# Performance work log

Measured on AMD Instinct MI355X. Metric: run time of the kernel, lower is better.

## Reference

```python
import jax, jax.numpy as jnp
import numpy as np

IMG = 1024       # original image resolution implied by (1024 - 1) normalization
STRIDE = 16
TEMP = 0.1
EPS = 1e-12      # F.normalize eps


def setup_inputs() -> dict:
    key = jax.random.key(0)
    k1, k2, k3, k4, k5 = jax.random.split(key, 5)
    B, C, Hf, Wf, N = 32, 256, 64, 64, 128
    feats_src = jax.random.normal(k1, (B, C, Hf, Wf), dtype=jnp.float32)
    feats_trg = jax.random.normal(k2, (B, C, Hf, Wf), dtype=jnp.float32)
    kps_src = jax.random.uniform(k3, (B, N, 2), dtype=jnp.float32) * (IMG - 1)
    kps_trg = jax.random.uniform(k4, (B, N, 2), dtype=jnp.float32) * (IMG - 1)
    kps_mask = jax.random.randint(k5, (B, N), 0, 2, dtype=jnp.int32)
    return {"feats_src": feats_src, "feats_trg": feats_trg,
            "kps_src": kps_src, "kps_trg": kps_trg, "kps_mask": kps_mask}


def _l2norm_c(x):
    # F.normalize(x, dim=1): x / max(||x||_2, eps) along channel dim
    n = jnp.sqrt(jnp.sum(x * x, axis=1, keepdims=True))
    return x / jnp.maximum(n, EPS)


def _bilinear_sample(feats, kps):
    # feats: [B,C,Hf,Wf]; kps: [B,N,2] pixel coords in [0, IMG-1]
    # Equivalent to F.grid_sample(align_corners=True, bilinear) with
    # grid = kps/(IMG-1)*2-1 -> pixel coords kps/(IMG-1)*(size-1).
    B, C, Hf, Wf = feats.shape
    x = kps[..., 0] / (IMG - 1) * (Wf - 1)  # [B,N]
    y = kps[..., 1] / (IMG - 1) * (Hf - 1)
    x0 = jnp.clip(jnp.floor(x), 0, Wf - 1).astype(jnp.int32)
    y0 = jnp.clip(jnp.floor(y), 0, Hf - 1).astype(jnp.int32)
    x1 = jnp.clip(x0 + 1, 0, Wf - 1)
    y1 = jnp.clip(y0 + 1, 0, Hf - 1)
    fx = x - x0.astype(x.dtype)
    fy = y - y0.astype(y.dtype)
    ft = jnp.transpose(feats, (0, 2, 3, 1))      # [B,Hf,Wf,C]
    bb = jnp.arange(B)[:, None]                  # [B,1] broadcasts to [B,N]
    g = lambda yy, xx: ft[bb, yy, xx]            # [B,N,C]
    wa = ((1 - fx) * (1 - fy))[..., None]
    wb = ((1 - fx) * fy)[..., None]
    wc = (fx * (1 - fy))[..., None]
    wd = (fx * fy)[..., None]
    return wa * g(y0, x0) + wb * g(y1, x0) + wc * g(y0, x1) + wd * g(y1, x1)


def reference(feats_src, feats_trg, kps_src, kps_trg, kps_mask):
    B, C, Hf, Wf = feats_src.shape
    N = kps_src.shape[1]
    fs = _l2norm_c(feats_src)
    ftg = _l2norm_c(feats_trg)

    # Query features sampled at source keypoints: [B,N,C]
    q = _bilinear_sample(fs, kps_src)

    # Logits over all target spatial positions: [B,N,Hf*Wf]
    trg_flat = ftg.reshape(B, C, Hf * Wf)
    logits = jnp.einsum('bnc,bcm->bnm', q, trg_flat) / TEMP

    # Bilinear soft targets at target keypoints (feature-grid coords)
    gx = kps_trg[..., 0] / STRIDE
    gy = kps_trg[..., 1] / STRIDE
    x0 = jnp.clip(jnp.floor(gx), 0, Wf - 1).astype(jnp.int32)
    x1 = jnp.clip(x0 + 1, 0, Wf - 1)
    y0 = jnp.clip(jnp.floor(gy), 0, Hf - 1).astype(jnp.int32)
    y1 = jnp.clip(y0 + 1, 0, Hf - 1)
    x0f, x1f = x0.astype(gx.dtype), x1.astype(gx.dtype)
    y0f, y1f = y0.astype(gy.dtype), y1.astype(gy.dtype)
    wa = (x1f - gx) * (y1f - gy)
    wb = (x1f - gx) * (gy - y0f)
    wc = (gx - x0f) * (y1f - gy)
    wd = (gx - x0f) * (gy - y0f)

    m = (kps_mask != 0).astype(logits.dtype)     # [B,N]
    w = jnp.stack([wa, wb, wc, wd], axis=-1) * m[..., None]   # [B,N,4]
    idx = jnp.stack([y0 * Wf + x0, y1 * Wf + x0,
                     y0 * Wf + x1, y1 * Wf + x1], axis=-1)    # [B,N,4]
    bb = jnp.arange(B)[:, None, None]
    nn = jnp.arange(N)[None, :, None]
    soft_targets = jnp.zeros_like(logits).at[bb, nn, idx].add(w)

    log_probs = jax.nn.log_softmax(logits, axis=-1)
    loss = -(soft_targets * log_probs).sum(axis=-1)           # [B,N]
    denom = jnp.maximum(m.sum(), 1.0)
    return (loss * m).sum() / denom
```

## Files before the change

### kernel.cpp

```cpp
#include <hip/hip_runtime.h>
#include <math.h>

#define B_    32
#define C_    256
#define HF    64
#define WF    64
#define M_    4096
#define N_    128
#define IMGM1 1023.0f
#define TEMP_ 0.1f
#define EPS_  1e-12f
#define NCH   32
#define SAS   40

typedef __attribute__((ext_vector_type(8))) short short8;
typedef __attribute__((ext_vector_type(4))) float floatx4;

__device__ __forceinline__ unsigned short f2bf(float x) {
  unsigned int u = __float_as_uint(x);
  u += 0x7fffu + ((u >> 16) & 1u);
  return (unsigned short)(u >> 16);
}
__device__ __forceinline__ float bf2f(unsigned short h) {
  return __uint_as_float(((unsigned int)h) << 16);
}
__device__ __forceinline__ float wave_sum(float v) {
#pragma unroll
  for (int off = 32; off; off >>= 1) v += __shfl_down(v, off, 64);
  return v;
}

__device__ __forceinline__ void src_geom(float kx, float ky, int& x0, int& y0,
                                         int& x1, int& y1, float& fx, float& fy) {
  const float x = kx / IMGM1 * (float)(WF - 1);
  const float y = ky / IMGM1 * (float)(HF - 1);
  x0 = (int)fminf(fmaxf(floorf(x), 0.f), 63.f);
  y0 = (int)fminf(fmaxf(floorf(y), 0.f), 63.f);
  x1 = min(x0 + 1, 63);
  y1 = min(y0 + 1, 63);
  fx = x - (float)x0;
  fy = y - (float)y0;
}

__global__ __launch_bounds__(256) void k1a_stage(const float* __restrict__ fs,
                                                 const float* __restrict__ kps,
                                                 ushort* __restrict__ corner,
                                                 float* __restrict__ ssqg) {
  const int cg = blockIdx.x, b = blockIdx.y, t = threadIdx.x;
  const int c0 = cg * 2;
  __shared__ __align__(16) float plane[2 * M_];
  __shared__ float4 ssq2[256];

  const float4* src = (const float4*)(fs + ((size_t)(b * C_ + c0)) * M_);
  float4* dst = (float4*)plane;
#pragma unroll
  for (int i = 0; i < 8; i++) dst[t + 256 * i] = src[t + 256 * i];
  __syncthreads();

  const int n = t & 127, p = t >> 7;
  const int c = c0 + p;
  const float kx = kps[((size_t)b * N_ + n) * 2 + 0];
  const float ky = kps[((size_t)b * N_ + n) * 2 + 1];
  int x0, y0, x1, y1; float fx, fy;
  src_geom(kx, ky, x0, y0, x1, y1, fx, fy);

  const float* pl = plane + p * M_;
  const float f00 = pl[y0 * WF + x0];
  const float f10 = pl[y1 * WF + x0];
  const float f01 = pl[y0 * WF + x1];
  const float f11 = pl[y1 * WF + x1];

  ushort4 cr;
  cr.x = f2bf(f00); cr.y = f2bf(f10); cr.z = f2bf(f01); cr.w = f2bf(f11);
  *(ushort4*)&corner[(((size_t)b * C_ + c) * N_ + n) * 4] = cr;

  ssq2[t] = make_float4(f00 * f00, f10 * f10, f01 * f01, f11 * f11);
  __syncthreads();
  if (t < 128) {
    const float4 a = ssq2[t], bq = ssq2[t + 128];
    float* g = ssqg + ((size_t)b * N_ + t) * 4;
    atomicAdd(g + 0, a.x + bq.x);
    atomicAdd(g + 1, a.y + bq.y);
    atomicAdd(g + 2, a.z + bq.z);
    atomicAdd(g + 3, a.w + bq.w);
  }
}

__global__ __launch_bounds__(256) void k1b_combine(const ushort* __restrict__ corner,
                                                   const float* __restrict__ ssqg,
                                                   const float* __restrict__ kps,
                                                   ushort* __restrict__ qbf) {
  const int n = blockIdx.x, b = blockIdx.y, c = threadIdx.x;
  const float kx = kps[((size_t)b * N_ + n) * 2 + 0];
  const float ky = kps[((size_t)b * N_ + n) * 2 + 1];
  int x0, y0, x1, y1; float fx, fy;
  src_geom(kx, ky, x0, y0, x1, y1, fx, fy);
  const float wa = (1.f - fx) * (1.f - fy), wb = (1.f - fx) * fy;
  const float wc = fx * (1.f - fy), wd = fx * fy;

  const float4 sq = *(const float4*)&ssqg[((size_t)b * N_ + n) * 4];
  const float r0 = 1.f / fmaxf(sqrtf(sq.x), EPS_);
  const float r1 = 1.f / fmaxf(sqrtf(sq.y), EPS_);
  const float r2 = 1.f / fmaxf(sqrtf(sq.z), EPS_);
  const float r3 = 1.f / fmaxf(sqrtf(sq.w), EPS_);

  const ushort4 cr = *(const ushort4*)&corner[(((size_t)b * C_ + c) * N_ + n) * 4];
  const float qv = wa * bf2f(cr.x) * r0 + wb * bf2f(cr.y) * r1 +
                   wc * bf2f(cr.z) * r2 + wd * bf2f(cr.w) * r3;
  qbf[((size_t)b * N_ + n) * C_ + c] = f2bf(qv);
}

__global__ __launch_bounds__(256) void k2_mfma(const float* __restrict__ trg,
                                               const ushort* __restrict__ qbf,
                                               const float* __restrict__ kps_trg,
                                               const int* __restrict__ mask,
                                               float2* __restrict__ part,
                                               float* __restrict__ tacc) {
  const int t = threadIdx.x;
  const int mb = blockIdx.x, b = blockIdx.y;
  const int m0 = mb * 128;
  const int wave = t >> 6, lane = t & 63;
  const int wn = wave >> 1, wm = wave & 1;
  const int lg = lane >> 4, ln = lane & 15;

  __shared__ __align__(16) short sA[128 * SAS];
  __shared__ __align__(16) short sB[128 * SAS];
  __shared__ __align__(16) float ssqp[16 * 128];
  __shared__ float scl[128];
  __shared__ float2 lser[128 * 2];
  __shared__ __align__(16) int   tidx[128][4];
  __shared__ __align__(16) float tw[128][4];

  floatx4 acc[4][4];
#pragma unroll
  for (int i = 0; i < 4; i++)
#pragma unroll
    for (int j = 0; j < 4; j++) acc[i][j] = (floatx4)0.f;

  float ssq[8];
#pragma unroll
  for (int e = 0; e < 8; e++) ssq[e] = 0.f;

  const ushort* qb = qbf + (size_t)b * N_ * C_;
  const float*  tb = trg + (size_t)b * C_ * M_ + m0;
  const int kk  = 2 * (t >> 4);
  const int m8  = (t & 15) * 8;
  const int gB  = kk >> 3;
  const int kin = kk & 7;

  for (int k0 = 0; k0 < C_; k0 += 32) {
#pragma unroll
    for (int l2 = 0; l2 < 2; l2++) {
      const int flat = t + 256 * l2;
      const int an = flat >> 2, ag = flat & 3;
      const short8 v = *(const short8*)(qb + an * C_ + k0 + ag * 8);
      *(short8*)&sA[an * SAS + ag * 8] = v;
    }
    {
      const float* p0 = tb + (size_t)(k0 + kk) * M_ + m8;
      const float* p1 = p0 + M_;
      const float4 a0 = *(const float4*)p0, a1 = *(const float4*)(p0 + 4);
      const float4 b0 = *(const float4*)p1, b1 = *(const float4*)(p1 + 4);
      const float v0[8] = {a0.x, a0.y, a0.z, a0.w, a1.x, a1.y, a1.z, a1.w};
      const float v1[8] = {b0.x, b0.y, b0.z, b0.w, b1.x, b1.y, b1.z, b1.w};
#pragma unroll
      for (int e = 0; e < 8; e++) {
        ssq[e] += v0[e] * v0[e] + v1[e] * v1[e];
        const int m = m8 + e;
        const int fm = (m >> 3) & 3;
        const unsigned int pr = (unsigned int)f2bf(v0[e]) | ((unsigned int)f2bf(v1[e]) << 16);
        *(unsigned int*)&sB[m * SAS + ((gB ^ fm) << 3) + kin] = pr;
      }
    }
    __syncthreads();
    short8 af[4], bfr[4];
#pragma unroll
    for (int i = 0; i < 4; i++)
      af[i] = *(const short8*)&sA[(wn * 64 + i * 16 + ln) * SAS + (lg << 3)];
#pragma unroll
    for (int j = 0; j < 4; j++) {
      const int m = wm * 64 + j * 16 + ln;
      const int fm = (m >> 3) & 3;
      bfr[j] = *(const short8*)&sB[m * SAS + ((lg ^ fm) << 3)];
    }
#pragma unroll
    for (int i = 0; i < 4; i++)
#pragma unroll
      for (int j = 0; j < 4; j++)
        acc[i][j] = __builtin_amdgcn_mfma_f32_16x16x32_bf16(af[i], bfr[j], acc[i][j], 0, 0, 0);
    __syncthreads();
  }

  *(float4*)&ssqp[(t >> 4) * 128 + m8]     = make_float4(ssq[0], ssq[1], ssq[2], ssq[3]);
  *(float4*)&ssqp[(t >> 4) * 128 + m8 + 4] = make_float4(ssq[4], ssq[5], ssq[6], ssq[7]);
  __syncthreads();
  if (t < 128) {
    float s = 0.f;
#pragma unroll
    for (int g = 0; g < 16; g++) s += ssqp[g * 128 + t];
    scl[t] = 1.f / (fmaxf(sqrtf(s), EPS_) * TEMP_);
    const float kx = kps_trg[((size_t)b * N_ + t) * 2 + 0];
    const float ky = kps_trg[((size_t)b * N_ + t) * 2 + 1];
    const float gx = kx * (1.f / 16.f), gy = ky * (1.f / 16.f);
    const int x0 = (int)fminf(fmaxf(floorf(gx), 0.f), 63.f);
    const int y0 = (int)fminf(fmaxf(floorf(gy), 0.f), 63.f);
    const int x1 = min(x0 + 1, 63), y1 = min(y0 + 1, 63);
    const float x0f = (float)x0, x1f = (float)x1, y0f = (float)y0, y1f = (float)y1;
    const float mk = (mask[(size_t)b * N_ + t] != 0) ? 1.f : 0.f;
    tidx[t][0] = y0 * WF + x0; tw[t][0] = (x1f - gx) * (y1f - gy) * mk;
    tidx[t][1] = y1 * WF + x0; tw[t][1] = (x1f - gx) * (gy - y0f) * mk;
    tidx[t][2] = y0 * WF + x1; tw[t][2] = (gx - x0f) * (y1f - gy) * mk;
    tidx[t][3] = y1 * WF + x1; tw[t][3] = (gx - x0f) * (gy - y0f) * mk;
  }
  __syncthreads();

  float scj[4];
#pragma unroll
  for (int j = 0; j < 4; j++) scj[j] = scl[wm * 64 + j * 16 + ln];
#pragma unroll
  for (int i = 0; i < 4; i++)
#pragma unroll
    for (int j = 0; j < 4; j++) acc[i][j] *= scj[j];

#pragma unroll
  for (int i = 0; i < 4; i++) {
#pragma unroll
    for (int r = 0; r < 4; r++) {
      float mx = fmaxf(fmaxf(acc[i][0][r], acc[i][1][r]), fmaxf(acc[i][2][r], acc[i][3][r]));
#pragma unroll
      for (int msk = 1; msk < 16; msk <<= 1) mx = fmaxf(mx, __shfl_xor(mx, msk, 64));
      float sm = __expf(acc[i][0][r] - mx) + __expf(acc[i][1][r] - mx) +
                 __expf(acc[i][2][r] - mx) + __expf(acc[i][3][r] - mx);
#pragma unroll
      for (int msk = 1; msk < 16; msk <<= 1) sm += __shfl_xor(sm, msk, 64);
      if (ln == 0) lser[(wn * 64 + i * 16 + lg * 4 + r) * 2 + wm] = make_float2(mx, sm);

      const int n = wn * 64 + i * 16 + lg * 4 + r;
      const int4  id4 = *(const int4*)&tidx[n][0];
      const float4 w4 = *(const float4*)&tw[n][0];
      const int   ida[4] = {id4.x, id4.y, id4.z, id4.w};
      const float wwa[4] = {w4.x, w4.y, w4.z, w4.w};
#pragma unroll
      for (int j = 0; j < 4; j++) {
        const int mg = m0 + wm * 64 + j * 16 + ln;
        const float lv = acc[i][j][r];
#pragma unroll
        for (int cc = 0; cc < 4; cc++)
          if (ida[cc] == mg && wwa[cc] != 0.f)
            atomicAdd(&tacc[(size_t)b * N_ + n], wwa[cc] * lv);
      }
    }
  }
  __syncthreads();
  if (t < 128) {
    const float2 u = lser[t * 2 + 0], v = lser[t * 2 + 1];
    const float M = fmaxf(u.x, v.x);
    const float S = u.y * __expf(u.x - M) + v.y * __expf(v.x - M);
    part[((size_t)b * N_ + t) * NCH + mb] = make_float2(M, S);
  }
}

__global__ __launch_bounds__(128) void k4_comb(const float2* __restrict__ part,
                                               const float* __restrict__ tacc,
                                               const float* __restrict__ kps_trg,
                                               const int* __restrict__ mask,
                                               float* __restrict__ gs) {
  const int b = blockIdx.x, t = threadIdx.x;
  const float2* p = part + ((size_t)b * N_ + t) * NCH;
  float M = -INFINITY;
#pragma unroll 8
  for (int c = 0; c < NCH; c++) M = fmaxf(M, p[c].x);
  float S = 0.f;
#pragma unroll 8
  for (int c = 0; c < NCH; c++) S += p[c].y * __expf(p[c].x - M);
  const float lse = M + logf(S);

  const float kx = kps_trg[((size_t)b * N_ + t) * 2 + 0];
  const float ky = kps_trg[((size_t)b * N_ + t) * 2 + 1];
  const float gx = kx * (1.f / 16.f), gy = ky * (1.f / 16.f);
  const int x0 = (int)fminf(fmaxf(floorf(gx), 0.f), 63.f);
  const int y0 = (int)fminf(fmaxf(floorf(gy), 0.f), 63.f);
  const int x1 = min(x0 + 1, 63), y1 = min(y0 + 1, 63);
  const float mk = (mask[(size_t)b * N_ + t] != 0) ? 1.f : 0.f;
  const float wsum = (float)(x1 - x0) * (float)(y1 - y0) * mk;

  float loss = wsum * lse - tacc[(size_t)b * N_ + t];
  float cnt = mk;
  loss = wave_sum(loss);
  cnt = wave_sum(cnt);
  __shared__ float sl[2], sc2[2];
  if ((t & 63) == 0) { sl[t >> 6] = loss; sc2[t >> 6] = cnt; }
  __syncthreads();
  if (t == 0) {
    atomicAdd(&gs[0], sl[0] + sl[1]);
    atomicAdd(&gs[1], sc2[0] + sc2[1]);
  }
}

__global__ void k5_final(const float* __restrict__ gs, float* __restrict__ out) {
  out[0] = gs[0] / fmaxf(gs[1], 1.f);
}

extern "C" void kernel_launch(void* const* d_in, const int* in_sizes, int n_in,
                              void* d_out, int out_size, void* d_ws, size_t ws_size,
                              hipStream_t stream) {
  const float* feats_src = (const float*)d_in[0];
  const float* feats_trg = (const float*)d_in[1];
  const float* kps_src   = (const float*)d_in[2];
  const float* kps_trg   = (const float*)d_in[3];
  const int*   kps_mask  = (const int*)d_in[4];
  float* out = (float*)d_out;

  char* wsb = (char*)d_ws;
  float*  ssqg   = (float*)(wsb + 0);
  float*  tacc   = (float*)(wsb + 65536);
  float*  gs     = (float*)(wsb + 81920);
  ushort* corner = (ushort*)(wsb + 82432);
  ushort* qbf    = (ushort*)(wsb + 8471040);
  float2* part   = (float2*)(wsb + 10568192);

  hipMemsetAsync(wsb, 0, 81928, stream);

  k1a_stage<<<dim3(C_ / 2, B_), 256, 0, stream>>>(feats_src, kps_src, corner, ssqg);
  k1b_combine<<<dim3(N_, B_), 256, 0, stream>>>(corner, ssqg, kps_src, qbf);
  k2_mfma<<<dim3(NCH, B_), 256, 0, stream>>>(feats_trg, qbf, kps_trg, kps_mask, part, tacc);
  k4_comb<<<dim3(B_), 128, 0, stream>>>(part, tacc, kps_trg, kps_mask, gs);
  k5_final<<<1, 1, 0, stream>>>(gs, out);
}
```

Baseline: 345.9 us.

## Pre-transpose target features to bf16 and stage GEMM tiles via direct global-to-LDS loads

Adds a new kernel that converts the fp32 target features into a bf16 [B,M,C] layout and precomputes the per-pixel inverse norms. The MFMA kernel then streams both operands with global_load_lds in 64-wide K chunks, using XOR swizzling, instead of converting fp32 to bf16 inside its inner loop. This takes the conversion and norm work off the GEMM loop. The cost is an extra pass that writes and then rereads a 64 MB bf16 buffer through global memory.

```diff
diff --git a/kernel.cpp b/kernel.cpp
--- a/kernel.cpp
+++ b/kernel.cpp
@@ -11,7 +11,8 @@
 #define TEMP_ 0.1f
 #define EPS_  1e-12f
 #define NCH   32
-#define SAS   40
+#define TCH   64
+#define BKK   64
 
 typedef __attribute__((ext_vector_type(8))) short short8;
 typedef __attribute__((ext_vector_type(4))) float floatx4;
@@ -28,6 +29,10 @@
 #pragma unroll
   for (int off = 32; off; off >>= 1) v += __shfl_down(v, off, 64);
   return v;
+}
+__device__ __forceinline__ void gl2lds16(const void* g, void* l) {
+  __builtin_amdgcn_global_load_lds((const __attribute__((address_space(1))) unsigned int*)g,
+                                   (__attribute__((address_space(3))) unsigned int*)l, 16, 0, 0);
 }
 
 __device__ __forceinline__ void src_geom(float kx, float ky, int& x0, int& y0,
@@ -40,6 +45,50 @@
   y1 = min(y0 + 1, 63);
   fx = x - (float)x0;
   fy = y - (float)y0;
+}
+
+__global__ __launch_bounds__(256) void k0_trgT(const float* __restrict__ trg,
+                                               ushort* __restrict__ trgT,
+                                               float* __restrict__ sclg) {
+  const int mb = blockIdx.x, b = blockIdx.y, t = threadIdx.x;
+  const int m0 = mb * TCH;
+  const int cr = t >> 5, ml = t & 31;
+  __shared__ unsigned int trdw[TCH * 129];
+  __shared__ float ssql[8][TCH];
+
+  ushort* trl = (ushort*)trdw;
+  const float* tb = trg + (size_t)b * C_ * M_ + m0;
+  float sq0 = 0.f, sq1 = 0.f;
+  for (int c0 = 0; c0 < C_; c0 += 8) {
+    const int c = c0 + cr;
+    const float v0 = tb[(size_t)c * M_ + ml];
+    const float v1 = tb[(size_t)c * M_ + ml + 32];
+    sq0 += v0 * v0;
+    sq1 += v1 * v1;
+    trl[ml * 258 + c] = f2bf(v0);
+    trl[(ml + 32) * 258 + c] = f2bf(v1);
+  }
+  ssql[cr][ml] = sq0;
+  ssql[cr][ml + 32] = sq1;
+  __syncthreads();
+  if (t < TCH) {
+    float s = 0.f;
+#pragma unroll
+    for (int r = 0; r < 8; r++) s += ssql[r][t];
+    sclg[(size_t)b * M_ + m0 + t] = 1.f / (fmaxf(sqrtf(s), EPS_) * TEMP_);
+  }
+  ushort* outb = trgT + ((size_t)b * M_ + m0) * C_;
+#pragma unroll
+  for (int it = 0; it < 8; it++) {
+    const int flat = it * 256 + t;
+    const int m = flat >> 5, ch = flat & 31;
+    uint4 d;
+    d.x = trdw[m * 129 + ch * 4 + 0];
+    d.y = trdw[m * 129 + ch * 4 + 1];
+    d.z = trdw[m * 129 + ch * 4 + 2];
+    d.w = trdw[m * 129 + ch * 4 + 3];
+    *(uint4*)&outb[(size_t)m * C_ + ch * 8] = d;
+  }
 }
 
 __global__ __launch_bounds__(256) void k1a_stage(const float* __restrict__ fs,
@@ -110,8 +159,9 @@
   qbf[((size_t)b * N_ + n) * C_ + c] = f2bf(qv);
 }
 
-__global__ __launch_bounds__(256) void k2_mfma(const float* __restrict__ trg,
+__global__ __launch_bounds__(256) void k2_mfma(const ushort* __restrict__ trgT,
                                                const ushort* __restrict__ qbf,
+                                               const float* __restrict__ sclg,
                                                const float* __restrict__ kps_trg,
                                                const int* __restrict__ mask,
                                                float2* __restrict__ part,
@@ -123,9 +173,8 @@
   const int wn = wave >> 1, wm = wave & 1;
   const int lg = lane >> 4, ln = lane & 15;
 
-  __shared__ __align__(16) short sA[128 * SAS];
-  __shared__ __align__(16) short sB[128 * SAS];
-  __shared__ __align__(16) float ssqp[16 * 128];
+  __shared__ __align__(16) short sA[128 * BKK];
+  __shared__ __align__(16) short sB[128 * BKK];
   __shared__ float scl[128];
   __shared__ float2 lser[128 * 2];
   __shared__ __align__(16) int   tidx[128][4];
@@ -137,68 +186,8 @@
 #pragma unroll
     for (int j = 0; j < 4; j++) acc[i][j] = (floatx4)0.f;
 
-  float ssq[8];
-#pragma unroll
-  for (int e = 0; e < 8; e++) ssq[e] = 0.f;
-
-  const ushort* qb = qbf + (size_t)b * N_ * C_;
-  const float*  tb = trg + (size_t)b * C_ * M_ + m0;
-  const int kk  = 2 * (t >> 4);
-  const int m8  = (t & 15) * 8;
-  const int gB  = kk >> 3;
-  const int kin = kk & 7;
-
-  for (int k0 = 0; k0 < C_; k0 += 32) {
-#pragma unroll
-    for (int l2 = 0; l2 < 2; l2++) {
-      const int flat = t + 256 * l2;
-      const int an = flat >> 2, ag = flat & 3;
-      const short8 v = *(const short8*)(qb + an * C_ + k0 + ag * 8);
-      *(short8*)&sA[an * SAS + ag * 8] = v;
-    }
-    {
-      const float* p0 = tb + (size_t)(k0 + kk) * M_ + m8;
-      const float* p1 = p0 + M_;
-      const float4 a0 = *(const float4*)p0, a1 = *(const float4*)(p0 + 4);
-      const float4 b0 = *(const float4*)p1, b1 = *(const float4*)(p1 + 4);
-      const float v0[8] = {a0.x, a0.y, a0.z, a0.w, a1.x, a1.y, a1.z, a1.w};
-      const float v1[8] = {b0.x, b0.y, b0.z, b0.w, b1.x, b1.y, b1.z, b1.w};
-#pragma unroll
-      for (int e = 0; e < 8; e++) {
-        ssq[e] += v0[e] * v0[e] + v1[e] * v1[e];
-        const int m = m8 + e;
-        const int fm = (m >> 3) & 3;
-        const unsigned int pr = (unsigned int)f2bf(v0[e]) | ((unsigned int)f2bf(v1[e]) << 16);
-        *(unsigned int*)&sB[m * SAS + ((gB ^ fm) << 3) + kin] = pr;
-      }
-    }
-    __syncthreads();
-    short8 af[4], bfr[4];
-#pragma unroll
-    for (int i = 0; i < 4; i++)
-      af[i] = *(const short8*)&sA[(wn * 64 + i * 16 + ln) * SAS + (lg << 3)];
-#pragma unroll
-    for (int j = 0; j < 4; j++) {
-      const int m = wm * 64 + j * 16 + ln;
-      const int fm = (m >> 3) & 3;
-      bfr[j] = *(const short8*)&sB[m * SAS + ((lg ^ fm) << 3)];
-    }
-#pragma unroll
-    for (int i = 0; i < 4; i++)
-#pragma unroll
-      for (int j = 0; j < 4; j++)
-        acc[i][j] = __builtin_amdgcn_mfma_f32_16x16x32_bf16(af[i], bfr[j], acc[i][j], 0, 0, 0);
-    __syncthreads();
-  }
-
-  *(float4*)&ssqp[(t >> 4) * 128 + m8]     = make_float4(ssq[0], ssq[1], ssq[2], ssq[3]);
-  *(float4*)&ssqp[(t >> 4) * 128 + m8 + 4] = make_float4(ssq[4], ssq[5], ssq[6], ssq[7]);
-  __syncthreads();
   if (t < 128) {
-    float s = 0.f;
-#pragma unroll
-    for (int g = 0; g < 16; g++) s += ssqp[g * 128 + t];
-    scl[t] = 1.f / (fmaxf(sqrtf(s), EPS_) * TEMP_);
+    scl[t] = sclg[(size_t)b * M_ + m0 + t];
     const float kx = kps_trg[((size_t)b * N_ + t) * 2 + 0];
     const float ky = kps_trg[((size_t)b * N_ + t) * 2 + 1];
     const float gx = kx * (1.f / 16.f), gy = ky * (1.f / 16.f);
@@ -212,7 +201,43 @@
     tidx[t][2] = y0 * WF + x1; tw[t][2] = (gx - x0f) * (y1f - gy) * mk;
     tidx[t][3] = y1 * WF + x1; tw[t][3] = (gx - x0f) * (gy - y0f) * mk;
   }
-  __syncthreads();
+
+  const char* qb = (const char*)(qbf + (size_t)b * N_ * C_);
+  const char* tb = (const char*)(trgT + ((size_t)b * M_ + m0) * C_);
+
+  for (int k0 = 0; k0 < C_; k0 += BKK) {
+#pragma unroll
+    for (int ii = 0; ii < 4; ii++) {
+      const int inst = wave * 4 + ii;
+      const int flat = inst * 64 + lane;
+      const int r = flat >> 3, cs = flat & 7;
+      const int clog = cs ^ (r & 7);
+      const int goff = r * 512 + k0 * 2 + clog * 16;
+      gl2lds16(qb + goff, &sA[inst * 512]);
+      gl2lds16(tb + goff, &sB[inst * 512]);
+    }
+    __syncthreads();
+#pragma unroll
+    for (int kk = 0; kk < 2; kk++) {
+      short8 af[4], bfr[4];
+#pragma unroll
+      for (int i = 0; i < 4; i++) {
+        const int n = wn * 64 + i * 16 + ln;
+        af[i] = *(const short8*)&sA[n * BKK + (((kk * 4 + lg) ^ (n & 7)) << 3)];
+      }
+#pragma unroll
+      for (int j = 0; j < 4; j++) {
+        const int m = wm * 64 + j * 16 + ln;
+        bfr[j] = *(const short8*)&sB[m * BKK + (((kk * 4 + lg) ^ (m & 7)) << 3)];
+      }
+#pragma unroll
+      for (int i = 0; i < 4; i++)
+#pragma unroll
+        for (int j = 0; j < 4; j++)
+          acc[i][j] = __builtin_amdgcn_mfma_f32_16x16x32_bf16(af[i], bfr[j], acc[i][j], 0, 0, 0);
+    }
+    __syncthreads();
+  }
 
   float scj[4];
 #pragma unroll
@@ -318,12 +343,15 @@
   ushort* corner = (ushort*)(wsb + 82432);
   ushort* qbf    = (ushort*)(wsb + 8471040);
   float2* part   = (float2*)(wsb + 10568192);
+  float*  sclg   = (float*)(wsb + 16777216);
+  ushort* trgT   = (ushort*)(wsb + 33554432);
 
   hipMemsetAsync(wsb, 0, 81928, stream);
 
+  k0_trgT<<<dim3(M_ / TCH, B_), 256, 0, stream>>>(feats_trg, trgT, sclg);
   k1a_stage<<<dim3(C_ / 2, B_), 256, 0, stream>>>(feats_src, kps_src, corner, ssqg);
   k1b_combine<<<dim3(N_, B_), 256, 0, stream>>>(corner, ssqg, kps_src, qbf);
-  k2_mfma<<<dim3(NCH, B_), 256, 0, stream>>>(feats_trg, qbf, kps_trg, kps_mask, part, tacc);
+  k2_mfma<<<dim3(NCH, B_), 256, 0, stream>>>(trgT, qbf, sclg, kps_trg, kps_mask, part, tacc);
   k4_comb<<<dim3(B_), 128, 0, stream>>>(part, tacc, kps_trg, kps_mask, gs);
   k5_final<<<1, 1, 0, stream>>>(gs, out);
 }
```

New measurement: 378.0 us. +9.3%, slower.

## Restructure similarity GEMM: full query tile in LDS, register-resident target operand

Applied to the files above, without the earlier changes.

The k2 kernel now loads the whole per-batch bf16 query matrix (128x256) into LDS once, using direct global-to-LDS loads with an XOR swizzle. Each wave streams its own 16-column slice of target features straight into registers, using a prefetched double-buffer and an in-register 4x4 shuffle transpose to build MFMA B fragments, so the staged sB tile and the per-k-step barriers go away. The M tile shrinks to 64, doubling the grid to 64x32 blocks, and per-column norms are reduced with wave shuffles instead of shared memory. In exchange it uses 64KB of LDS per block, which limits occupancy, and it doubles the partial softmax entries the combine kernel has to read.

```diff
diff --git a/kernel.cpp b/kernel.cpp
--- a/kernel.cpp
+++ b/kernel.cpp
@@ -10,8 +10,8 @@
 #define IMGM1 1023.0f
 #define TEMP_ 0.1f
 #define EPS_  1e-12f
-#define NCH   32
-#define SAS   40
+#define BM2   64
+#define NMB   (M_ / BM2)
 
 typedef __attribute__((ext_vector_type(8))) short short8;
 typedef __attribute__((ext_vector_type(4))) float floatx4;
@@ -28,6 +28,26 @@
 #pragma unroll
   for (int off = 32; off; off >>= 1) v += __shfl_down(v, off, 64);
   return v;
+}
+__device__ __forceinline__ void gl2lds16(const void* g, void* l) {
+  __builtin_amdgcn_global_load_lds((const __attribute__((address_space(1))) unsigned int*)g,
+                                   (__attribute__((address_space(3))) unsigned int*)l, 16, 0, 0);
+}
+__device__ __forceinline__ float4 shflx4(float4 v, int m) {
+  float4 r;
+  r.x = __shfl_xor(v.x, m, 64);
+  r.y = __shfl_xor(v.y, m, 64);
+  r.z = __shfl_xor(v.z, m, 64);
+  r.w = __shfl_xor(v.w, m, 64);
+  return r;
+}
+__device__ __forceinline__ float4 t4x4(float4 v, int e) {
+  float4 p = shflx4(v, 1);
+  float4 w = ((e & 1) == 0) ? make_float4(v.x, p.x, v.z, p.z)
+                            : make_float4(p.y, v.y, p.w, v.w);
+  float4 p2 = shflx4(w, 2);
+  return ((e & 2) == 0) ? make_float4(w.x, w.y, p2.x, p2.y)
+                        : make_float4(p2.z, p2.w, w.z, w.w);
 }
 
 __device__ __forceinline__ void src_geom(float kx, float ky, int& x0, int& y0,
@@ -118,87 +138,26 @@
                                                float* __restrict__ tacc) {
   const int t = threadIdx.x;
   const int mb = blockIdx.x, b = blockIdx.y;
-  const int m0 = mb * 128;
   const int wave = t >> 6, lane = t & 63;
-  const int wn = wave >> 1, wm = wave & 1;
-  const int lg = lane >> 4, ln = lane & 15;
-
-  __shared__ __align__(16) short sA[128 * SAS];
-  __shared__ __align__(16) short sB[128 * SAS];
-  __shared__ __align__(16) float ssqp[16 * 128];
-  __shared__ float scl[128];
-  __shared__ float2 lser[128 * 2];
+  const int lg = lane >> 4;
+  const int q4 = (lane >> 2) & 3;
+  const int e  = lane & 3;
+  const int ln = lane & 15;
+
+  __shared__ __align__(16) ushort qlds[N_ * C_];
+  __shared__ float2 lred[128][4];
   __shared__ __align__(16) int   tidx[128][4];
   __shared__ __align__(16) float tw[128][4];
 
-  floatx4 acc[4][4];
-#pragma unroll
-  for (int i = 0; i < 4; i++)
-#pragma unroll
-    for (int j = 0; j < 4; j++) acc[i][j] = (floatx4)0.f;
-
-  float ssq[8];
-#pragma unroll
-  for (int e = 0; e < 8; e++) ssq[e] = 0.f;
-
-  const ushort* qb = qbf + (size_t)b * N_ * C_;
-  const float*  tb = trg + (size_t)b * C_ * M_ + m0;
-  const int kk  = 2 * (t >> 4);
-  const int m8  = (t & 15) * 8;
-  const int gB  = kk >> 3;
-  const int kin = kk & 7;
-
-  for (int k0 = 0; k0 < C_; k0 += 32) {
-#pragma unroll
-    for (int l2 = 0; l2 < 2; l2++) {
-      const int flat = t + 256 * l2;
-      const int an = flat >> 2, ag = flat & 3;
-      const short8 v = *(const short8*)(qb + an * C_ + k0 + ag * 8);
-      *(short8*)&sA[an * SAS + ag * 8] = v;
-    }
-    {
-      const float* p0 = tb + (size_t)(k0 + kk) * M_ + m8;
-      const float* p1 = p0 + M_;
-      const float4 a0 = *(const float4*)p0, a1 = *(const float4*)(p0 + 4);
-      const float4 b0 = *(const float4*)p1, b1 = *(const float4*)(p1 + 4);
-      const float v0[8] = {a0.x, a0.y, a0.z, a0.w, a1.x, a1.y, a1.z, a1.w};
-      const float v1[8] = {b0.x, b0.y, b0.z, b0.w, b1.x, b1.y, b1.z, b1.w};
-#pragma unroll
-      for (int e = 0; e < 8; e++) {
-        ssq[e] += v0[e] * v0[e] + v1[e] * v1[e];
-        const int m = m8 + e;
-        const int fm = (m >> 3) & 3;
-        const unsigned int pr = (unsigned int)f2bf(v0[e]) | ((unsigned int)f2bf(v1[e]) << 16);
-        *(unsigned int*)&sB[m * SAS + ((gB ^ fm) << 3) + kin] = pr;
-      }
-    }
-    __syncthreads();
-    short8 af[4], bfr[4];
-#pragma unroll
-    for (int i = 0; i < 4; i++)
-      af[i] = *(const short8*)&sA[(wn * 64 + i * 16 + ln) * SAS + (lg << 3)];
-#pragma unroll
-    for (int j = 0; j < 4; j++) {
-      const int m = wm * 64 + j * 16 + ln;
-      const int fm = (m >> 3) & 3;
-      bfr[j] = *(const short8*)&sB[m * SAS + ((lg ^ fm) << 3)];
-    }
-#pragma unroll
-    for (int i = 0; i < 4; i++)
-#pragma unroll
-      for (int j = 0; j < 4; j++)
-        acc[i][j] = __builtin_amdgcn_mfma_f32_16x16x32_bf16(af[i], bfr[j], acc[i][j], 0, 0, 0);
-    __syncthreads();
-  }
-
-  *(float4*)&ssqp[(t >> 4) * 128 + m8]     = make_float4(ssq[0], ssq[1], ssq[2], ssq[3]);
-  *(float4*)&ssqp[(t >> 4) * 128 + m8 + 4] = make_float4(ssq[4], ssq[5], ssq[6], ssq[7]);
-  __syncthreads();
+  const char* qb = (const char*)(qbf + (size_t)b * N_ * C_);
+#pragma unroll
+  for (int it = 0; it < 16; it++) {
+    const int flat = it * 256 + t;
+    const int r = flat >> 5, cs = flat & 31;
+    gl2lds16(qb + r * 512 + ((cs ^ (r & 7)) << 4),
+             (char*)qlds + (it * 256 + wave * 64) * 16);
+  }
   if (t < 128) {
-    float s = 0.f;
-#pragma unroll
-    for (int g = 0; g < 16; g++) s += ssqp[g * 128 + t];
-    scl[t] = 1.f / (fmaxf(sqrtf(s), EPS_) * TEMP_);
     const float kx = kps_trg[((size_t)b * N_ + t) * 2 + 0];
     const float ky = kps_trg[((size_t)b * N_ + t) * 2 + 1];
     const float gx = kx * (1.f / 16.f), gy = ky * (1.f / 16.f);
@@ -214,49 +173,87 @@
   }
   __syncthreads();
 
-  float scj[4];
-#pragma unroll
-  for (int j = 0; j < 4; j++) scj[j] = scl[wm * 64 + j * 16 + ln];
-#pragma unroll
-  for (int i = 0; i < 4; i++)
-#pragma unroll
-    for (int j = 0; j < 4; j++) acc[i][j] *= scj[j];
-
-#pragma unroll
-  for (int i = 0; i < 4; i++) {
+  floatx4 acc[8];
+#pragma unroll
+  for (int i = 0; i < 8; i++) acc[i] = (floatx4)0.f;
+  float4 ssq4 = make_float4(0.f, 0.f, 0.f, 0.f);
+
+  const float* pl = trg + (size_t)b * C_ * M_ + (size_t)(lg * 8 + e) * M_ +
+                    mb * BM2 + wave * 16 + q4 * 4;
+
+  float4 L0 = *(const float4*)pl;
+  float4 L1 = *(const float4*)(pl + 4 * M_);
+#pragma unroll
+  for (int s = 0; s < 8; s++) {
+    float4 N0 = L0, N1 = L1;
+    if (s < 7) {
+      N0 = *(const float4*)(pl + (size_t)(s + 1) * 32 * M_);
+      N1 = *(const float4*)(pl + (size_t)((s + 1) * 32 + 4) * M_);
+    }
+    ssq4.x += L0.x * L0.x + L1.x * L1.x;
+    ssq4.y += L0.y * L0.y + L1.y * L1.y;
+    ssq4.z += L0.z * L0.z + L1.z * L1.z;
+    ssq4.w += L0.w * L0.w + L1.w * L1.w;
+
+    const float4 T0 = t4x4(L0, e);
+    const float4 T1 = t4x4(L1, e);
+    short8 bfr;
+    bfr[0] = (short)f2bf(T0.x); bfr[1] = (short)f2bf(T0.y);
+    bfr[2] = (short)f2bf(T0.z); bfr[3] = (short)f2bf(T0.w);
+    bfr[4] = (short)f2bf(T1.x); bfr[5] = (short)f2bf(T1.y);
+    bfr[6] = (short)f2bf(T1.z); bfr[7] = (short)f2bf(T1.w);
+
+#pragma unroll
+    for (int i = 0; i < 8; i++) {
+      const int row = i * 16 + ln;
+      const int ch = (s * 4 + lg) ^ (row & 7);
+      const short8 af = *(const short8*)&qlds[row * 256 + (ch << 3)];
+      acc[i] = __builtin_amdgcn_mfma_f32_16x16x32_bf16(af, bfr, acc[i], 0, 0, 0);
+    }
+    L0 = N0; L1 = N1;
+  }
+
+#pragma unroll
+  for (int m = 0; m < 4; m++) {
+    const int msk = (m < 2) ? (1 << m) : (16 << (m - 2));
+    const float4 o = shflx4(ssq4, msk);
+    ssq4.x += o.x; ssq4.y += o.y; ssq4.z += o.z; ssq4.w += o.w;
+  }
+  const float tt = (e == 0) ? ssq4.x : (e == 1) ? ssq4.y : (e == 2) ? ssq4.z : ssq4.w;
+  const float scl = 1.f / (fmaxf(sqrtf(tt), EPS_) * TEMP_);
+#pragma unroll
+  for (int i = 0; i < 8; i++) acc[i] *= scl;
+
+  const int mglob = mb * BM2 + wave * 16 + ln;
+#pragma unroll
+  for (int i = 0; i < 8; i++) {
 #pragma unroll
     for (int r = 0; r < 4; r++) {
-      float mx = fmaxf(fmaxf(acc[i][0][r], acc[i][1][r]), fmaxf(acc[i][2][r], acc[i][3][r]));
+      const float val = acc[i][r];
+      float mx = val;
 #pragma unroll
       for (int msk = 1; msk < 16; msk <<= 1) mx = fmaxf(mx, __shfl_xor(mx, msk, 64));
-      float sm = __expf(acc[i][0][r] - mx) + __expf(acc[i][1][r] - mx) +
-                 __expf(acc[i][2][r] - mx) + __expf(acc[i][3][r] - mx);
+      float sm = __expf(val - mx);
 #pragma unroll
       for (int msk = 1; msk < 16; msk <<= 1) sm += __shfl_xor(sm, msk, 64);
-      if (ln == 0) lser[(wn * 64 + i * 16 + lg * 4 + r) * 2 + wm] = make_float2(mx, sm);
-
-      const int n = wn * 64 + i * 16 + lg * 4 + r;
-      const int4  id4 = *(const int4*)&tidx[n][0];
-      const float4 w4 = *(const float4*)&tw[n][0];
-      const int   ida[4] = {id4.x, id4.y, id4.z, id4.w};
-      const float wwa[4] = {w4.x, w4.y, w4.z, w4.w};
-#pragma unroll
-      for (int j = 0; j < 4; j++) {
-        const int mg = m0 + wm * 64 + j * 16 + ln;
-        const float lv = acc[i][j][r];
-#pragma unroll
-        for (int cc = 0; cc < 4; cc++)
-          if (ida[cc] == mg && wwa[cc] != 0.f)
-            atomicAdd(&tacc[(size_t)b * N_ + n], wwa[cc] * lv);
-      }
+      const int nrow = i * 16 + lg * 4 + r;
+      if (ln == 0) lred[nrow][wave] = make_float2(mx, sm);
+
+      const int4  id4 = *(const int4*)&tidx[nrow][0];
+      const float4 w4 = *(const float4*)&tw[nrow][0];
+      if (id4.x == mglob && w4.x != 0.f) atomicAdd(&tacc[(size_t)b * N_ + nrow], w4.x * val);
+      if (id4.y == mglob && w4.y != 0.f) atomicAdd(&tacc[(size_t)b * N_ + nrow], w4.y * val);
+      if (id4.z == mglob && w4.z != 0.f) atomicAdd(&tacc[(size_t)b * N_ + nrow], w4.z * val);
+      if (id4.w == mglob && w4.w != 0.f) atomicAdd(&tacc[(size_t)b * N_ + nrow], w4.w * val);
     }
   }
   __syncthreads();
   if (t < 128) {
-    const float2 u = lser[t * 2 + 0], v = lser[t * 2 + 1];
-    const float M = fmaxf(u.x, v.x);
-    const float S = u.y * __expf(u.x - M) + v.y * __expf(v.x - M);
-    part[((size_t)b * N_ + t) * NCH + mb] = make_float2(M, S);
+    const float2 a = lred[t][0], bq = lred[t][1], c = lred[t][2], d = lred[t][3];
+    float M = fmaxf(fmaxf(a.x, bq.x), fmaxf(c.x, d.x));
+    float S = a.y * __expf(a.x - M) + bq.y * __expf(bq.x - M) +
+              c.y * __expf(c.x - M) + d.y * __expf(d.x - M);
+    part[((size_t)b * N_ + t) * NMB + mb] = make_float2(M, S);
   }
 }
 
@@ -266,13 +263,13 @@
                                                const int* __restrict__ mask,
                                                float* __restrict__ gs) {
   const int b = blockIdx.x, t = threadIdx.x;
-  const float2* p = part + ((size_t)b * N_ + t) * NCH;
+  const float2* p = part + ((size_t)b * N_ + t) * NMB;
   float M = -INFINITY;
 #pragma unroll 8
-  for (int c = 0; c < NCH; c++) M = fmaxf(M, p[c].x);
+  for (int c = 0; c < NMB; c++) M = fmaxf(M, p[c].x);
   float S = 0.f;
 #pragma unroll 8
-  for (int c = 0; c < NCH; c++) S += p[c].y * __expf(p[c].x - M);
+  for (int c = 0; c < NMB; c++) S += p[c].y * __expf(p[c].x - M);
   const float lse = M + logf(S);
 
   const float kx = kps_trg[((size_t)b * N_ + t) * 2 + 0];
@@ -323,7 +320,7 @@
 
   k1a_stage<<<dim3(C_ / 2, B_), 256, 0, stream>>>(feats_src, kps_src, corner, ssqg);
   k1b_combine<<<dim3(N_, B_), 256, 0, stream>>>(corner, ssqg, kps_src, qbf);
-  k2_mfma<<<dim3(NCH, B_), 256, 0, stream>>>(feats_trg, qbf, kps_trg, kps_mask, part, tacc);
+  k2_mfma<<<dim3(NMB, B_), 256, 0, stream>>>(feats_trg, qbf, kps_trg, kps_mask, part, tacc);
   k4_comb<<<dim3(B_), 128, 0, stream>>>(part, tacc, kps_trg, kps_mask, gs);
   k5_final<<<1, 1, 0, stream>>>(gs, out);
 }
```

New measurement: 381.2 us. 10.2% more time.
